# Optimization experiments

Hardware: AMD Instinct MI355X
Metric: run time of the kernel (lower is better)

Reference implementation:

```python
import jax, jax.numpy as jnp
import numpy as np

EPS = 1e-5


def _interp_conv(x, pos_in, pos_out, idx, w1, b1, w2, b2, kernel, bias):
    # x: [B, Cin, Nin]; idx: [Nout, K] neighbor indices into the input grid.
    off = pos_in[idx] - pos_out[:, None, :]            # [Nout, K, 2] relative offsets
    h = jax.nn.relu(off @ w1 + b1)                     # [Nout, K, 16] weight-net hidden
    A = h @ w2 + b2                                    # [Nout, K, T] interp weights onto T kernel taps
    feat = x[:, :, idx]                                # [B, Cin, Nout, K] irregular gather
    taps = jnp.einsum('bcnk,nkt->bcnt', feat, A)       # resample neighbors onto canonical taps
    return jnp.einsum('bcnt,oct->bon', taps, kernel) + bias[None, :, None]


def _bn_relu(x, g, b):
    # BatchNorm1d (training-style batch stats over (B, N)) + ReLU
    m = x.mean(axis=(0, 2), keepdims=True)
    v = x.var(axis=(0, 2), keepdims=True)
    return jax.nn.relu((x - m) * jax.lax.rsqrt(v + EPS) * g[None, :, None] + b[None, :, None])


def setup_inputs():
    key = jax.random.key(0)
    ks = jax.random.split(key, 24)
    B, N1, N2, N3, K, T = 16, 50176, 12544, 3136, 9, 9
    d = {}
    d['x'] = jax.random.normal(ks[0], (B, 3, N1), jnp.float32)
    d['l1'] = jax.random.uniform(ks[1], (N1, 2), jnp.float32)
    d['l2'] = jax.random.uniform(ks[2], (N2, 2), jnp.float32)
    d['l3'] = jax.random.uniform(ks[3], (N3, 2), jnp.float32)
    d['knn1'] = jax.random.randint(ks[4], (N2, K), 0, N1)
    d['knn2'] = jax.random.randint(ks[5], (N2, K), 0, N2)
    d['knn3'] = jax.random.randint(ks[6], (N2, K), 0, N2)
    d['pool_idx'] = jax.random.randint(ks[7], (N3, 4), 0, N2)
    cins = {'c1': 3, 'c2': 32, 'c3': 32}
    couts = {'c1': 32, 'c2': 32, 'c3': 64}
    for i, p in enumerate(['c1', 'c2', 'c3']):
        d[p + '_wn_w1'] = jax.random.normal(ks[8 + 4 * i], (2, 16), jnp.float32) * 0.5
        d[p + '_wn_b1'] = jnp.zeros(16, jnp.float32)
        d[p + '_wn_w2'] = jax.random.normal(ks[9 + 4 * i], (16, T), jnp.float32) * 0.3
        d[p + '_wn_b2'] = jnp.zeros(T, jnp.float32)
        d[p + '_kernel'] = jax.random.normal(ks[10 + 4 * i], (couts[p], cins[p], T), jnp.float32) * np.float32(1.0 / np.sqrt(cins[p] * T))
        d[p + '_bias'] = jnp.zeros(couts[p], jnp.float32)
    for p, c in [('bn1', 32), ('bn2', 32), ('bn3', 64)]:
        d[p + '_g'] = jnp.ones(c, jnp.float32)
        d[p + '_b'] = jnp.zeros(c, jnp.float32)
    return d


def reference(x, l1, l2, l3, knn1, knn2, knn3, pool_idx,
              c1_wn_w1, c1_wn_b1, c1_wn_w2, c1_wn_b2, c1_kernel, c1_bias,
              c2_wn_w1, c2_wn_b1, c2_wn_w2, c2_wn_b2, c2_kernel, c2_bias,
              c3_wn_w1, c3_wn_b1, c3_wn_w2, c3_wn_b2, c3_kernel, c3_bias,
              bn1_g, bn1_b, bn2_g, bn2_b, bn3_g, bn3_b):
    h = _interp_conv(x, l1, l2, knn1, c1_wn_w1, c1_wn_b1, c1_wn_w2, c1_wn_b2, c1_kernel, c1_bias)
    h = _bn_relu(h, bn1_g, bn1_b)
    h = _interp_conv(h, l2, l2, knn2, c2_wn_w1, c2_wn_b1, c2_wn_w2, c2_wn_b2, c2_kernel, c2_bias)
    h = _bn_relu(h, bn2_g, bn2_b)
    h = _interp_conv(h, l2, l2, knn3, c3_wn_w1, c3_wn_b1, c3_wn_w2, c3_wn_b2, c3_kernel, c3_bias)
    h = _bn_relu(h, bn3_g, bn3_b)
    # MaxPoolNG: max over 4 nearest neighbors on the non-uniform grid -> [B, 64, N3]
    return h[:, :, pool_idx].max(axis=-1)
```

## Files before the change

### kernel.cpp

```cpp
#include <hip/hip_runtime.h>
#include <hip/hip_bf16.h>
#include <cfloat>

#define N1C 50176
#define N2C 12544
#define N3C 3136

typedef __attribute__((ext_vector_type(8))) short short8v;
typedef __attribute__((ext_vector_type(4))) float f32x4;

static __device__ __forceinline__ unsigned short f2bf(float f){
  __hip_bfloat16 h = __float2bfloat16(f);
  return *reinterpret_cast<unsigned short*>(&h);
}
static __device__ __forceinline__ float bflo(unsigned v){
  return __uint_as_float(v << 16);
}
static __device__ __forceinline__ float bfhi(unsigned v){
  return __uint_as_float(v & 0xFFFF0000u);
}
static __device__ __forceinline__ float bf2f(unsigned short u){
  return __uint_as_float(((unsigned)u) << 16);
}

__global__ __launch_bounds__(256) void transpose_x_kernel(
    const float* __restrict__ x, unsigned short* __restrict__ xTb)
{
  __shared__ float tile[48][65];
  int n0 = blockIdx.x * 64;
  int tid = threadIdx.x;
  int i = tid & 63;
  for (int rr = tid >> 6; rr < 48; rr += 4)
    tile[rr][i] = x[(size_t)rr * N1C + n0 + i];
  __syncthreads();
  for (int j = tid; j < 64*64; j += 256){
    int ii = j >> 6, bc = j & 63, b = bc >> 2, c = bc & 3;
    float v = (c < 3) ? tile[b*3 + c][ii] : 0.f;
    xTb[(size_t)n0 * 64 + j] = f2bf(v);
  }
}

__global__ __launch_bounds__(256) void compute_A_kernel(
    const float* __restrict__ pos_in, const float* __restrict__ pos_out,
    const int* __restrict__ idx,
    const float* __restrict__ w1, const float* __restrict__ b1,
    const float* __restrict__ w2, const float* __restrict__ b2,
    float* __restrict__ Abuf)
{
  int g = blockIdx.x * 256 + threadIdx.x;
  if (g >= N2C * 9) return;
  int n = g / 9;
  int p = idx[g];
  float o0 = pos_in[2*p]   - pos_out[2*n];
  float o1 = pos_in[2*p+1] - pos_out[2*n+1];
  float A[9];
  #pragma unroll
  for (int t = 0; t < 9; t++) A[t] = b2[t];
  #pragma unroll
  for (int j = 0; j < 16; j++){
    float h = fmaxf(fmaf(o0, w1[j], fmaf(o1, w1[16+j], b1[j])), 0.f);
    #pragma unroll
    for (int t = 0; t < 9; t++) A[t] = fmaf(h, w2[j*9 + t], A[t]);
  }
  #pragma unroll
  for (int t = 0; t < 9; t++) Abuf[(size_t)g*9 + t] = A[t];
}

__global__ __launch_bounds__(256) void wcvt_kernel(
    const float* __restrict__ W, unsigned short* __restrict__ Wb,
    int total, int K, int KW)
{
  int i = blockIdx.x * 256 + threadIdx.x;
  if (i >= total) return;
  int o = i / KW, k = i % KW;
  Wb[i] = f2bf(k < K ? W[o*K + k] : 0.f);
}

template<int CIN, int CINP, int COUT, int NPB, bool AFFINE>
__global__ __launch_bounds__(256) void conv_mfma_kernel(
    const unsigned short* __restrict__ in, const int* __restrict__ idx,
    const float* __restrict__ Abuf, const unsigned short* __restrict__ Wb,
    const float* __restrict__ bias,
    const float* __restrict__ scale, const float* __restrict__ shift,
    unsigned short* __restrict__ out, float* __restrict__ gpart)
{
  constexpr int K    = CIN * 9;
  constexpr int KW   = (K < 32) ? 32 : K;
  constexpr int KROW = (K < 32) ? 48 : 296;
  constexpr int CHUNKS = KW / 32;
  constexpr int OT   = COUT / 16;
  constexpr int HP   = CINP / 2;
  constexpr int PPT  = 16 * HP;

  __shared__ alignas(16) unsigned short Tb[NPB * 16 * KROW];
  __shared__ float As[NPB * 81];
  __shared__ int   Ip[NPB * 9];
  __shared__ float Sw[4 * COUT];
  __shared__ float Sq[4 * COUT];

  int n0 = blockIdx.x * NPB;
  int tid = threadIdx.x;
  for (int i = tid; i < NPB*81; i += 256) As[i] = Abuf[(size_t)n0*81 + i];
  if (tid < NPB*9) Ip[tid] = idx[n0*9 + tid];
  for (int i = tid; i < 4*COUT; i += 256){ Sw[i] = 0.f; Sq[i] = 0.f; }
  if (K < 32){
    for (int i = tid; i < NPB*16*KROW/2; i += 256) ((unsigned*)Tb)[i] = 0u;
  }
  __syncthreads();

  for (int u = tid; u < NPB*PPT; u += 256){
    int ni = u / PPT, loc = u % PPT;
    int b = loc / HP, c2 = loc % HP;
    const float* As_n = As + ni*81;
    const int*   ip   = Ip + ni*9;
    float scx=1.f, shx=0.f, scy=1.f, shy=0.f;
    if (AFFINE){
      scx = scale[2*c2];   shx = shift[2*c2];
      scy = scale[2*c2+1]; shy = shift[2*c2+1];
    }
    float fx[9], fy[9];
    #pragma unroll
    for (int k = 0; k < 9; k++){
      unsigned v = *(const unsigned*)(in + ((size_t)ip[k]*16 + b)*CINP + 2*c2);
      float x0 = bflo(v), y0 = bfhi(v);
      if (AFFINE){
        x0 = fmaxf(fmaf(x0, scx, shx), 0.f);
        y0 = fmaxf(fmaf(y0, scy, shy), 0.f);
      }
      fx[k] = x0; fy[k] = y0;
    }
    unsigned short e[18];
    #pragma unroll
    for (int t = 0; t < 9; t++){
      float s0 = 0.f, s1 = 0.f;
      #pragma unroll
      for (int k = 0; k < 9; k++){
        float a = As_n[k*9 + t];
        s0 = fmaf(fx[k], a, s0);
        s1 = fmaf(fy[k], a, s1);
      }
      e[t] = f2bf(s0); e[9+t] = f2bf(s1);
    }
    unsigned* dst = (unsigned*)(Tb + (ni*16 + b)*KROW + 18*c2);
    #pragma unroll
    for (int j = 0; j < 9; j++) dst[j] = (unsigned)e[2*j] | ((unsigned)e[2*j+1] << 16);
  }
  __syncthreads();

  int w = tid >> 6, l = tid & 63, lr = l & 15, lg = l >> 4;
  float smr[4] = {0,0,0,0}, sqr[4] = {0,0,0,0};
  int oBase = 0;
  for (int wi = w; wi < NPB*OT; wi += 4){
    int ni = wi / OT, ot = wi % OT;
    oBase = 16*ot + 4*lg;
    f32x4 acc;
    #pragma unroll
    for (int r = 0; r < 4; r++) acc[r] = bias[oBase + r];
    const short8v* ap = (const short8v*)(Wb + (size_t)(16*ot + lr)*KW) + lg;
    const short8v* bp = (const short8v*)(Tb + (ni*16 + lr)*KROW) + lg;
    #pragma unroll
    for (int kk = 0; kk < CHUNKS; kk++)
      acc = __builtin_amdgcn_mfma_f32_16x16x32_bf16(ap[kk*4], bp[kk*4], acc, 0, 0, 0);
    ushort4 o4;
    o4.x = f2bf(acc[0]); o4.y = f2bf(acc[1]); o4.z = f2bf(acc[2]); o4.w = f2bf(acc[3]);
    *(ushort4*)(out + ((size_t)(n0 + ni)*16 + lr)*COUT + oBase) = o4;
    #pragma unroll
    for (int r = 0; r < 4; r++){
      smr[r] += acc[r];
      sqr[r] = fmaf(acc[r], acc[r], sqr[r]);
    }
  }
  #pragma unroll
  for (int m = 1; m < 16; m <<= 1){
    #pragma unroll
    for (int r = 0; r < 4; r++){
      smr[r] += __shfl_xor(smr[r], m);
      sqr[r] += __shfl_xor(sqr[r], m);
    }
  }
  if (lr == 0){
    #pragma unroll
    for (int r = 0; r < 4; r++){
      Sw[w*COUT + oBase + r] = smr[r];
      Sq[w*COUT + oBase + r] = sqr[r];
    }
  }
  __syncthreads();
  for (int o = tid; o < COUT; o += 256){
    float sm = Sw[o] + Sw[COUT + o] + Sw[2*COUT + o] + Sw[3*COUT + o];
    float sq = Sq[o] + Sq[COUT + o] + Sq[2*COUT + o] + Sq[3*COUT + o];
    gpart[(size_t)blockIdx.x * 2*COUT + o] = sm;
    gpart[(size_t)blockIdx.x * 2*COUT + COUT + o] = sq;
  }
}

template<int COUT>
__global__ __launch_bounds__(256, 4) void conv_wave_kernel(
    const unsigned short* __restrict__ in, const int* __restrict__ idx,
    const float* __restrict__ Abuf, const unsigned short* __restrict__ Wb,
    const float* __restrict__ bias,
    const float* __restrict__ scale, const float* __restrict__ shift,
    unsigned short* __restrict__ out, float* __restrict__ gpart)
{
  constexpr int NPB  = 4;
  constexpr int KROW = 296;
  constexpr int OT   = COUT / 16;

  __shared__ alignas(16) unsigned short Tb[NPB * 16 * KROW];
  __shared__ float Sw[4 * COUT];
  __shared__ float Sq[4 * COUT];
  __shared__ float Ssc[32], Ssh[32];

  int tid = threadIdx.x;
  int w = tid >> 6, l = tid & 63;
  int n0 = blockIdx.x * NPB;
  if (tid < 32){ Ssc[tid] = scale[tid]; Ssh[tid] = shift[tid]; }
  for (int i = tid; i < 4*COUT; i += 256){ Sw[i] = 0.f; Sq[i] = 0.f; }
  __syncthreads();

  int nws = __builtin_amdgcn_readfirstlane(n0 + w);

  float areg[81];
  {
    const float* Ap = Abuf + (size_t)nws * 81;
    #pragma unroll
    for (int j = 0; j < 81; j++) areg[j] = Ap[j];
  }
  int ip[9];
  {
    const int* ipr = idx + nws * 9;
    #pragma unroll
    for (int k = 0; k < 9; k++) ip[k] = ipr[k];
  }

  int b = l & 15, cg = l >> 4;
  float scv[8], shv[8];
  #pragma unroll
  for (int p = 0; p < 8; p++){ scv[p] = Ssc[cg*8 + p]; shv[p] = Ssh[cg*8 + p]; }

  uint4 rv[9];
  #pragma unroll
  for (int k = 0; k < 9; k++){
    const unsigned short* rp = in + (size_t)ip[k]*512 + b*32 + cg*8;
    rv[k] = *(const uint4*)rp;
  }

  float acc[72];
  #pragma unroll
  for (int i = 0; i < 72; i++) acc[i] = 0.f;
  #pragma unroll
  for (int k = 0; k < 9; k++){
    unsigned uu[4] = {rv[k].x, rv[k].y, rv[k].z, rv[k].w};
    #pragma unroll
    for (int p = 0; p < 4; p++){
      float x0 = fmaxf(fmaf(bflo(uu[p]), scv[2*p],   shv[2*p]),   0.f);
      float y0 = fmaxf(fmaf(bfhi(uu[p]), scv[2*p+1], shv[2*p+1]), 0.f);
      #pragma unroll
      for (int t = 0; t < 9; t++){
        float a = areg[k*9 + t];
        acc[(2*p)*9 + t]   = fmaf(x0, a, acc[(2*p)*9 + t]);
        acc[(2*p+1)*9 + t] = fmaf(y0, a, acc[(2*p+1)*9 + t]);
      }
    }
  }
  uint4* dst4 = (uint4*)(Tb + (w*16 + b)*KROW + cg*72);
  #pragma unroll
  for (int q = 0; q < 9; q++){
    uint4 o;
    o.x = (unsigned)f2bf(acc[8*q+0]) | ((unsigned)f2bf(acc[8*q+1]) << 16);
    o.y = (unsigned)f2bf(acc[8*q+2]) | ((unsigned)f2bf(acc[8*q+3]) << 16);
    o.z = (unsigned)f2bf(acc[8*q+4]) | ((unsigned)f2bf(acc[8*q+5]) << 16);
    o.w = (unsigned)f2bf(acc[8*q+6]) | ((unsigned)f2bf(acc[8*q+7]) << 16);
    dst4[q] = o;
  }
  __syncthreads();

  int lr = l & 15, lg = l >> 4;
  float smr[4] = {0,0,0,0}, sqr[4] = {0,0,0,0};
  int oBase = 0;
  for (int wi = w; wi < NPB*OT; wi += 4){
    int ni = wi / OT, ot = wi % OT;
    oBase = 16*ot + 4*lg;
    f32x4 acc3;
    #pragma unroll
    for (int r = 0; r < 4; r++) acc3[r] = bias[oBase + r];
    const short8v* ap = (const short8v*)(Wb + (size_t)(16*ot + lr)*288) + lg;
    const short8v* bp = (const short8v*)(Tb + (ni*16 + lr)*KROW) + lg;
    #pragma unroll
    for (int kk = 0; kk < 9; kk++)
      acc3 = __builtin_amdgcn_mfma_f32_16x16x32_bf16(ap[kk*4], bp[kk*4], acc3, 0, 0, 0);
    ushort4 o4;
    o4.x = f2bf(acc3[0]); o4.y = f2bf(acc3[1]); o4.z = f2bf(acc3[2]); o4.w = f2bf(acc3[3]);
    *(ushort4*)(out + ((size_t)(n0 + ni)*16 + lr)*COUT + oBase) = o4;
    #pragma unroll
    for (int r = 0; r < 4; r++){
      smr[r] += acc3[r];
      sqr[r] = fmaf(acc3[r], acc3[r], sqr[r]);
    }
  }
  #pragma unroll
  for (int m = 1; m < 16; m <<= 1){
    #pragma unroll
    for (int r = 0; r < 4; r++){
      smr[r] += __shfl_xor(smr[r], m);
      sqr[r] += __shfl_xor(sqr[r], m);
    }
  }
  if (lr == 0){
    #pragma unroll
    for (int r = 0; r < 4; r++){
      Sw[w*COUT + oBase + r] = smr[r];
      Sq[w*COUT + oBase + r] = sqr[r];
    }
  }
  __syncthreads();
  for (int o = tid; o < COUT; o += 256){
    float sm = Sw[o] + Sw[COUT + o] + Sw[2*COUT + o] + Sw[3*COUT + o];
    float sq = Sq[o] + Sq[COUT + o] + Sq[2*COUT + o] + Sq[3*COUT + o];
    gpart[(size_t)blockIdx.x * 2*COUT + o] = sm;
    gpart[(size_t)blockIdx.x * 2*COUT + COUT + o] = sq;
  }
}

__global__ __launch_bounds__(256) void bn_finalize_kernel(
    const float* __restrict__ gpart, int NB, int C,
    const float* __restrict__ g, const float* __restrict__ bb,
    float* __restrict__ sc, float* __restrict__ sh, float invN)
{
  int c = blockIdx.x;
  float sm = 0.f, sq = 0.f;
  for (int i = threadIdx.x; i < NB; i += 256){
    sm += gpart[(size_t)i*2*C + c];
    sq += gpart[(size_t)i*2*C + C + c];
  }
  #pragma unroll
  for (int off = 32; off > 0; off >>= 1){
    sm += __shfl_down(sm, off);
    sq += __shfl_down(sq, off);
  }
  __shared__ float rs[8];
  int wd = threadIdx.x >> 6, ln = threadIdx.x & 63;
  if (ln == 0){ rs[wd] = sm; rs[4+wd] = sq; }
  __syncthreads();
  if (threadIdx.x == 0){
    float S = rs[0]+rs[1]+rs[2]+rs[3], Q = rs[4]+rs[5]+rs[6]+rs[7];
    float mean = S * invN;
    float var  = fmaxf(Q * invN - mean*mean, 0.f);
    float s = g[c] * rsqrtf(var + 1e-5f);
    sc[c] = s;
    sh[c] = bb[c] - mean * s;
  }
}

__global__ __launch_bounds__(256) void pool_kernel(
    const unsigned short* __restrict__ h3, const int* __restrict__ pidx,
    const float* __restrict__ sc, const float* __restrict__ sh,
    float* __restrict__ out)
{
  __shared__ float P[16][1024];
  int m0 = blockIdx.x * 16;
  int tid = threadIdx.x;
  for (int mi = 0; mi < 16; mi++){
    int m = m0 + mi;
    int p0 = pidx[m*4+0], p1 = pidx[m*4+1], p2 = pidx[m*4+2], p3 = pidx[m*4+3];
    #pragma unroll
    for (int q = 0; q < 4; q++){
      int bo = tid + q*256;
      int o = bo & 63;
      float s = sc[o], h = sh[o];
      float v0 = fmaf(bf2f(h3[(size_t)p0*1024 + bo]), s, h);
      float v1 = fmaf(bf2f(h3[(size_t)p1*1024 + bo]), s, h);
      float v2 = fmaf(bf2f(h3[(size_t)p2*1024 + bo]), s, h);
      float v3 = fmaf(bf2f(h3[(size_t)p3*1024 + bo]), s, h);
      P[mi][bo] = fmaxf(fmaxf(fmaxf(v0,v1), fmaxf(v2,v3)), 0.f);
    }
  }
  __syncthreads();
  #pragma unroll
  for (int w = 0; w < 4; w++){
    int r = tid + w*256;
    float* dst = out + (size_t)r*N3C + m0;
    #pragma unroll
    for (int mi = 0; mi < 16; mi++) dst[mi] = P[mi][r];
  }
}

extern "C" void kernel_launch(void* const* d_in, const int* in_sizes, int n_in,
                              void* d_out, int out_size, void* d_ws, size_t ws_size,
                              hipStream_t stream)
{
  const float* x    = (const float*)d_in[0];
  const float* l1   = (const float*)d_in[1];
  const float* l2   = (const float*)d_in[2];
  const int* knn1   = (const int*)d_in[4];
  const int* knn2   = (const int*)d_in[5];
  const int* knn3   = (const int*)d_in[6];
  const int* pidx   = (const int*)d_in[7];

  const float* c1_w1 = (const float*)d_in[8];
  const float* c1_b1 = (const float*)d_in[9];
  const float* c1_w2 = (const float*)d_in[10];
  const float* c1_b2 = (const float*)d_in[11];
  const float* c1_k  = (const float*)d_in[12];
  const float* c1_bs = (const float*)d_in[13];
  const float* c2_w1 = (const float*)d_in[14];
  const float* c2_b1 = (const float*)d_in[15];
  const float* c2_w2 = (const float*)d_in[16];
  const float* c2_b2 = (const float*)d_in[17];
  const float* c2_k  = (const float*)d_in[18];
  const float* c2_bs = (const float*)d_in[19];
  const float* c3_w1 = (const float*)d_in[20];
  const float* c3_b1 = (const float*)d_in[21];
  const float* c3_w2 = (const float*)d_in[22];
  const float* c3_b2 = (const float*)d_in[23];
  const float* c3_k  = (const float*)d_in[24];
  const float* c3_bs = (const float*)d_in[25];
  const float* bn1_g = (const float*)d_in[26];
  const float* bn1_b = (const float*)d_in[27];
  const float* bn2_g = (const float*)d_in[28];
  const float* bn2_b = (const float*)d_in[29];
  const float* bn3_g = (const float*)d_in[30];
  const float* bn3_b = (const float*)d_in[31];

  char* ws = (char*)d_ws;
  unsigned short* xTb = (unsigned short*)(ws + 0);
  unsigned short* h1  = (unsigned short*)(ws + 6422528);
  unsigned short* h2  = (unsigned short*)(ws + 19267584);
  unsigned short* h3  = (unsigned short*)(ws + 32112640);
  float* Abuf         = (float*)(ws + 57802752);
  float* gpart        = (float*)(ws + 61867008);
  unsigned short* wb1 = (unsigned short*)(ws + 65078272);
  unsigned short* wb2 = (unsigned short*)(ws + 65081344);
  unsigned short* wb3 = (unsigned short*)(ws + 65099776);
  float* sc1 = (float*)(ws + 65137664); float* sh1 = sc1 + 32;
  float* sc2 = sh1 + 32;                float* sh2 = sc2 + 32;
  float* sc3 = sh2 + 32;                float* sh3 = sc3 + 64;

  const float invN = 1.0f / (float)(N2C * 16);
  const int ablocks = (N2C * 9 + 255) / 256;

  transpose_x_kernel<<<N1C/64, 256, 0, stream>>>(x, xTb);
  wcvt_kernel<<<(32*32 + 255)/256, 256, 0, stream>>>(c1_k, wb1, 32*32, 27, 32);
  wcvt_kernel<<<(32*288 + 255)/256, 256, 0, stream>>>(c2_k, wb2, 32*288, 288, 288);
  wcvt_kernel<<<(64*288 + 255)/256, 256, 0, stream>>>(c3_k, wb3, 64*288, 288, 288);

  compute_A_kernel<<<ablocks, 256, 0, stream>>>(l1, l2, knn1, c1_w1, c1_b1, c1_w2, c1_b2, Abuf);
  conv_mfma_kernel<3, 4, 32, 8, false><<<N2C/8, 256, 0, stream>>>(
      xTb, knn1, Abuf, wb1, c1_bs, nullptr, nullptr, h1, gpart);
  bn_finalize_kernel<<<32, 256, 0, stream>>>(gpart, N2C/8, 32, bn1_g, bn1_b, sc1, sh1, invN);

  compute_A_kernel<<<ablocks, 256, 0, stream>>>(l2, l2, knn2, c2_w1, c2_b1, c2_w2, c2_b2, Abuf);
  conv_wave_kernel<32><<<N2C/4, 256, 0, stream>>>(
      h1, knn2, Abuf, wb2, c2_bs, sc1, sh1, h2, gpart);
  bn_finalize_kernel<<<32, 256, 0, stream>>>(gpart, N2C/4, 32, bn2_g, bn2_b, sc2, sh2, invN);

  compute_A_kernel<<<ablocks, 256, 0, stream>>>(l2, l2, knn3, c3_w1, c3_b1, c3_w2, c3_b2, Abuf);
  conv_wave_kernel<64><<<N2C/4, 256, 0, stream>>>(
      h2, knn3, Abuf, wb3, c3_bs, sc2, sh2, h3, gpart);
  bn_finalize_kernel<<<64, 256, 0, stream>>>(gpart, N2C/4, 64, bn3_g, bn3_b, sc3, sh3, invN);

  pool_kernel<<<N3C/16, 256, 0, stream>>>(h3, pidx, sc3, sh3, (float*)d_out);
}
```

Baseline: 175.9 us.

## Split interp accumulation into halves and give each wave its own point's MFMA

The tap-resampling stage now runs in two halves of 36 accumulators instead of 72, which cuts register pressure to support the 4-blocks-per-CU launch bound. Scale and shift are read straight from global memory as float4 instead of being staged in shared memory, which removes the initial barrier. Each wave now runs the MFMA output stage only on its own point's LDS rows, which drops the block-wide barrier between the tap write and the matmul. BN partial sums are reduced per output tile with shuffles, adding more shuffle work in exchange.

Result: faster. 169.2 us (-3.8%).

```diff
diff --git a/kernel.cpp b/kernel.cpp
--- a/kernel.cpp
+++ b/kernel.cpp
@@ -209,14 +209,10 @@
   __shared__ alignas(16) unsigned short Tb[NPB * 16 * KROW];
   __shared__ float Sw[4 * COUT];
   __shared__ float Sq[4 * COUT];
-  __shared__ float Ssc[32], Ssh[32];
 
   int tid = threadIdx.x;
   int w = tid >> 6, l = tid & 63;
   int n0 = blockIdx.x * NPB;
-  if (tid < 32){ Ssc[tid] = scale[tid]; Ssh[tid] = shift[tid]; }
-  for (int i = tid; i < 4*COUT; i += 256){ Sw[i] = 0.f; Sq[i] = 0.f; }
-  __syncthreads();
 
   int nws = __builtin_amdgcn_readfirstlane(n0 + w);
 
@@ -234,9 +230,10 @@
   }
 
   int b = l & 15, cg = l >> 4;
-  float scv[8], shv[8];
-  #pragma unroll
-  for (int p = 0; p < 8; p++){ scv[p] = Ssc[cg*8 + p]; shv[p] = Ssh[cg*8 + p]; }
+  float4 scA = *(const float4*)(scale + cg*8);
+  float4 scB = *(const float4*)(scale + cg*8 + 4);
+  float4 shA = *(const float4*)(shift + cg*8);
+  float4 shB = *(const float4*)(shift + cg*8 + 4);
 
   uint4 rv[9];
   #pragma unroll
@@ -245,72 +242,79 @@
     rv[k] = *(const uint4*)rp;
   }
 
-  float acc[72];
-  #pragma unroll
-  for (int i = 0; i < 72; i++) acc[i] = 0.f;
-  #pragma unroll
-  for (int k = 0; k < 9; k++){
-    unsigned uu[4] = {rv[k].x, rv[k].y, rv[k].z, rv[k].w};
-    #pragma unroll
-    for (int p = 0; p < 4; p++){
-      float x0 = fmaxf(fmaf(bflo(uu[p]), scv[2*p],   shv[2*p]),   0.f);
-      float y0 = fmaxf(fmaf(bfhi(uu[p]), scv[2*p+1], shv[2*p+1]), 0.f);
+  #pragma unroll
+  for (int h = 0; h < 2; h++){
+    float sc[4], sh[4];
+    if (h == 0){
+      sc[0]=scA.x; sc[1]=scA.y; sc[2]=scA.z; sc[3]=scA.w;
+      sh[0]=shA.x; sh[1]=shA.y; sh[2]=shA.z; sh[3]=shA.w;
+    } else {
+      sc[0]=scB.x; sc[1]=scB.y; sc[2]=scB.z; sc[3]=scB.w;
+      sh[0]=shB.x; sh[1]=shB.y; sh[2]=shB.z; sh[3]=shB.w;
+    }
+    float acc[36];
+    #pragma unroll
+    for (int i = 0; i < 36; i++) acc[i] = 0.f;
+    #pragma unroll
+    for (int k = 0; k < 9; k++){
+      unsigned u0 = (h == 0) ? rv[k].x : rv[k].z;
+      unsigned u1 = (h == 0) ? rv[k].y : rv[k].w;
+      float c0 = fmaxf(fmaf(bflo(u0), sc[0], sh[0]), 0.f);
+      float c1 = fmaxf(fmaf(bfhi(u0), sc[1], sh[1]), 0.f);
+      float c2 = fmaxf(fmaf(bflo(u1), sc[2], sh[2]), 0.f);
+      float c3 = fmaxf(fmaf(bfhi(u1), sc[3], sh[3]), 0.f);
       #pragma unroll
       for (int t = 0; t < 9; t++){
         float a = areg[k*9 + t];
-        acc[(2*p)*9 + t]   = fmaf(x0, a, acc[(2*p)*9 + t]);
-        acc[(2*p+1)*9 + t] = fmaf(y0, a, acc[(2*p+1)*9 + t]);
+        acc[t]      = fmaf(c0, a, acc[t]);
+        acc[9 + t]  = fmaf(c1, a, acc[9 + t]);
+        acc[18 + t] = fmaf(c2, a, acc[18 + t]);
+        acc[27 + t] = fmaf(c3, a, acc[27 + t]);
       }
     }
-  }
-  uint4* dst4 = (uint4*)(Tb + (w*16 + b)*KROW + cg*72);
-  #pragma unroll
-  for (int q = 0; q < 9; q++){
-    uint4 o;
-    o.x = (unsigned)f2bf(acc[8*q+0]) | ((unsigned)f2bf(acc[8*q+1]) << 16);
-    o.y = (unsigned)f2bf(acc[8*q+2]) | ((unsigned)f2bf(acc[8*q+3]) << 16);
-    o.z = (unsigned)f2bf(acc[8*q+4]) | ((unsigned)f2bf(acc[8*q+5]) << 16);
-    o.w = (unsigned)f2bf(acc[8*q+6]) | ((unsigned)f2bf(acc[8*q+7]) << 16);
-    dst4[q] = o;
-  }
-  __syncthreads();
+    uint2* du = (uint2*)(Tb + (size_t)(w*16 + b)*KROW + cg*72 + h*36);
+    #pragma unroll
+    for (int q = 0; q < 9; q++){
+      uint2 o;
+      o.x = (unsigned)f2bf(acc[4*q+0]) | ((unsigned)f2bf(acc[4*q+1]) << 16);
+      o.y = (unsigned)f2bf(acc[4*q+2]) | ((unsigned)f2bf(acc[4*q+3]) << 16);
+      du[q] = o;
+    }
+  }
 
   int lr = l & 15, lg = l >> 4;
-  float smr[4] = {0,0,0,0}, sqr[4] = {0,0,0,0};
-  int oBase = 0;
-  for (int wi = w; wi < NPB*OT; wi += 4){
-    int ni = wi / OT, ot = wi % OT;
-    oBase = 16*ot + 4*lg;
-    f32x4 acc3;
-    #pragma unroll
-    for (int r = 0; r < 4; r++) acc3[r] = bias[oBase + r];
+  const short8v* bp = (const short8v*)(Tb + (size_t)(w*16 + lr)*KROW) + lg;
+  #pragma unroll
+  for (int ot = 0; ot < OT; ot++){
+    int oBase = 16*ot + 4*lg;
+    f32x4 a3;
+    #pragma unroll
+    for (int r = 0; r < 4; r++) a3[r] = bias[oBase + r];
     const short8v* ap = (const short8v*)(Wb + (size_t)(16*ot + lr)*288) + lg;
-    const short8v* bp = (const short8v*)(Tb + (ni*16 + lr)*KROW) + lg;
     #pragma unroll
     for (int kk = 0; kk < 9; kk++)
-      acc3 = __builtin_amdgcn_mfma_f32_16x16x32_bf16(ap[kk*4], bp[kk*4], acc3, 0, 0, 0);
+      a3 = __builtin_amdgcn_mfma_f32_16x16x32_bf16(ap[kk*4], bp[kk*4], a3, 0, 0, 0);
     ushort4 o4;
-    o4.x = f2bf(acc3[0]); o4.y = f2bf(acc3[1]); o4.z = f2bf(acc3[2]); o4.w = f2bf(acc3[3]);
-    *(ushort4*)(out + ((size_t)(n0 + ni)*16 + lr)*COUT + oBase) = o4;
-    #pragma unroll
-    for (int r = 0; r < 4; r++){
-      smr[r] += acc3[r];
-      sqr[r] = fmaf(acc3[r], acc3[r], sqr[r]);
-    }
-  }
-  #pragma unroll
-  for (int m = 1; m < 16; m <<= 1){
-    #pragma unroll
-    for (int r = 0; r < 4; r++){
-      smr[r] += __shfl_xor(smr[r], m);
-      sqr[r] += __shfl_xor(sqr[r], m);
-    }
-  }
-  if (lr == 0){
-    #pragma unroll
-    for (int r = 0; r < 4; r++){
-      Sw[w*COUT + oBase + r] = smr[r];
-      Sq[w*COUT + oBase + r] = sqr[r];
+    o4.x = f2bf(a3[0]); o4.y = f2bf(a3[1]); o4.z = f2bf(a3[2]); o4.w = f2bf(a3[3]);
+    *(ushort4*)(out + ((size_t)(n0 + w)*16 + lr)*COUT + oBase) = o4;
+
+    float smr[4], sqr[4];
+    #pragma unroll
+    for (int r = 0; r < 4; r++){ smr[r] = a3[r]; sqr[r] = a3[r]*a3[r]; }
+    #pragma unroll
+    for (int m = 1; m < 16; m <<= 1){
+      #pragma unroll
+      for (int r = 0; r < 4; r++){
+        smr[r] += __shfl_xor(smr[r], m);
+        sqr[r] += __shfl_xor(sqr[r], m);
+      }
+    }
+    if (lr == 0){
+      #pragma unroll
+      for (int r = 0; r < 4; r++){
+        Sw[w*COUT + oBase + r] = smr[r];
+        Sq[w*COUT + oBase + r] = sqr[r];
+      }
     }
   }
   __syncthreads();
```
